# Kernel tuning notes

Hardware: AMD Instinct MI355X
Metric: run time of the kernel (lower is better)

The kernel has to match this reference:

```python
import jax, jax.numpy as jnp
import numpy as np

B, L, H = 32, 2048, 1024  # batch, seq (atoms), hid_dim; trg last dim = 3*H


def setup_inputs() -> dict:
    key = jax.random.key(0)
    k1, k2, k3, k4 = jax.random.split(key, 4)
    trg = jax.random.normal(k1, (B, L, 3 * H), dtype=jnp.float32)
    src = jax.random.normal(k2, (B, 512, H), dtype=jnp.float32)  # unused (n_layers=0)
    fc_w = jax.random.normal(k3, (H, 3 * H), dtype=jnp.float32) * (1.0 / np.sqrt(3 * H))
    fc_b = jax.random.normal(k4, (H,), dtype=jnp.float32) * 0.01
    return {"trg": trg, "src": src, "fc_w": fc_w, "fc_b": fc_b}


def reference(trg, src, fc_w, fc_b):
    # decoder layers: n_layers == 0 -> identity
    t = jnp.einsum('blk,hk->blh', trg, fc_w) + fc_b          # fc: [B, L, H]
    norm1 = jnp.linalg.norm(t, axis=2)                        # [B, L]
    w = jax.nn.softmax(norm1, axis=1)                         # [B, L]
    # vectorized form of the nested python-loop weighted-sum pooling
    summ = jnp.einsum('blh,bl->bh', t, w)                     # [B, H]
    return (summ, norm1)
```

## Files before the change

kernel.cpp:

```cpp
#include <hip/hip_runtime.h>
#include <hip/hip_bf16.h>


#define B_ 32
#define L_ 2048
#define H_ 1024
#define K_ 3072
#define M_ 65536

typedef __attribute__((ext_vector_type(8))) short short8;
typedef __attribute__((ext_vector_type(4))) float floatx4;

__device__ __forceinline__ unsigned int pack_bf16x2(float a, float b) {
    __hip_bfloat162 h = __float22bfloat162_rn(make_float2(a, b));
    return *reinterpret_cast<unsigned int*>(&h);
}

__device__ __forceinline__ float bf2f(unsigned short u) {
    return __uint_as_float(((unsigned int)u) << 16);
}

__device__ __forceinline__ void gl_lds16(const unsigned short* g, unsigned short* l) {
    __builtin_amdgcn_global_load_lds(
        (const __attribute__((address_space(1))) unsigned int*)g,
        (__attribute__((address_space(3))) unsigned int*)l, 16, 0, 0);
}

__global__ void __launch_bounds__(256) convert_bf16_kernel(const float* __restrict__ in,
                                                           unsigned short* __restrict__ out,
                                                           int n8) {
    int i = blockIdx.x * blockDim.x + threadIdx.x;
    const int stride = gridDim.x * blockDim.x;
    for (; i < n8; i += stride) {
        const float4* pp = (const float4*)in + (size_t)i * 2;
        float4 a = pp[0], b = pp[1];
        uint4 r;
        r.x = pack_bf16x2(a.x, a.y);
        r.y = pack_bf16x2(a.z, a.w);
        r.z = pack_bf16x2(b.x, b.y);
        r.w = pack_bf16x2(b.z, b.w);
        ((uint4*)out)[i] = r;
    }
}

__global__ void __launch_bounds__(256, 4) gemm_norm_bf_kernel(
        const unsigned short* __restrict__ A,
        const unsigned short* __restrict__ Bw,
        const float* __restrict__ fcb,
        float* __restrict__ normsq) {
    __shared__ unsigned short As[128 * 32];
    __shared__ unsigned short Bs[128 * 32];

    const int tid = threadIdx.x;
    const int bid = blockIdx.x;
    const int group  = bid >> 6;
    const int lane64 = bid & 63;
    const int xcd    = lane64 & 7;
    const int nblk   = lane64 >> 3;
    const int mblk   = group * 8 + xcd;
    const int R0 = mblk * 128;
    const int N0 = nblk * 128;

    const int wv = tid >> 6, lane = tid & 63;
    const int wr = wv >> 1, wc = wv & 1;
    const int q = lane >> 4, ln = lane & 15;

    const int r0    = wv * 32;
    const int lrow  = lane >> 2;
    const int lchnk = lane & 3;
    const unsigned short* agp = A  + (size_t)(R0 + r0 + lrow) * K_ + lchnk * 8;
    const unsigned short* bgp = Bw + (size_t)(N0 + r0 + lrow) * K_ + lchnk * 8;
    unsigned short* alds0 = &As[r0 * 32];
    unsigned short* alds1 = &As[(r0 + 16) * 32];
    unsigned short* blds0 = &Bs[r0 * 32];
    unsigned short* blds1 = &Bs[(r0 + 16) * 32];
    const size_t roff = (size_t)16 * K_;

    gl_lds16(agp, alds0);
    gl_lds16(agp + roff, alds1);
    gl_lds16(bgp, blds0);
    gl_lds16(bgp + roff, blds1);

    floatx4 acc[4][4] = {};
    const unsigned short* Af = &As[(wr * 64 + ln) * 32 + q * 8];
    const unsigned short* Bf = &Bs[(wc * 64 + ln) * 32 + q * 8];

    for (int step = 0; step < 96; ++step) {
        __syncthreads();

        short8 af[4], bf[4];
#pragma unroll
        for (int i = 0; i < 4; ++i) {
            af[i] = *(const short8*)(Af + i * 16 * 32);
            bf[i] = *(const short8*)(Bf + i * 16 * 32);
        }

        __syncthreads();

        if (step < 95) {
            const int kk = (step + 1) * 32;
            gl_lds16(agp + kk, alds0);
            gl_lds16(agp + roff + kk, alds1);
            gl_lds16(bgp + kk, blds0);
            gl_lds16(bgp + roff + kk, blds1);
        }

#pragma unroll
        for (int mi = 0; mi < 4; ++mi)
#pragma unroll
            for (int ni = 0; ni < 4; ++ni)
                acc[mi][ni] = __builtin_amdgcn_mfma_f32_16x16x32_bf16(af[mi], bf[ni],
                                                                      acc[mi][ni], 0, 0, 0);
    }

    float bz[4];
#pragma unroll
    for (int ni = 0; ni < 4; ++ni) bz[ni] = fcb[N0 + wc * 64 + ni * 16 + ln];

    float* nsq = normsq + R0 + wr * 64;
#pragma unroll
    for (int mi = 0; mi < 4; ++mi) {
#pragma unroll
        for (int r = 0; r < 4; ++r) {
            float s = 0.0f;
#pragma unroll
            for (int ni = 0; ni < 4; ++ni) {
                float v = acc[mi][ni][r] + bz[ni];
                s += v * v;
            }
            s += __shfl_xor(s, 1);
            s += __shfl_xor(s, 2);
            s += __shfl_xor(s, 4);
            s += __shfl_xor(s, 8);
            if (ln == 0) atomicAdd(&nsq[mi * 16 + q * 4 + r], s);
        }
    }
}

#define LDST 40
__global__ void __launch_bounds__(256) gemm_norm_f32_kernel(const float* __restrict__ trg,
                                                            const float* __restrict__ fcw,
                                                            const float* __restrict__ fcb,
                                                            float* __restrict__ normsq) {
    __shared__ unsigned short As[128 * LDST];
    __shared__ unsigned short Bs[128 * LDST];

    const int tid  = threadIdx.x;
    const int bid  = blockIdx.x;
    const int group  = bid >> 6;
    const int lane64 = bid & 63;
    const int nblk   = lane64 >> 3;
    const int mblk   = group * 8 + (lane64 & 7);
    const int R0   = mblk * 128;
    const int N0   = nblk * 128;
    const int wv   = tid >> 6;
    const int lane = tid & 63;
    const int wr   = wv >> 1;
    const int wc   = wv & 1;
    const int q    = lane >> 4;
    const int ln   = lane & 15;

    floatx4 acc[4][4] = {};

    const int srow = tid >> 3;
    const int skc  = tid & 7;
    const float* ap = trg + (size_t)(R0 + srow) * K_ + skc * 4;
    const float* bp = fcw + (size_t)(N0 + srow) * K_ + skc * 4;
    unsigned short* AsW = &As[srow * LDST + skc * 4];
    unsigned short* BsW = &Bs[srow * LDST + skc * 4];

    const unsigned short* Af = &As[(wr * 64 + ln) * LDST + q * 8];
    const unsigned short* Bf = &Bs[(wc * 64 + ln) * LDST + q * 8];

    float4 ra[4], rb[4];
#pragma unroll
    for (int s = 0; s < 4; ++s) {
        ra[s] = *(const float4*)(ap + (size_t)(s * 32) * K_);
        rb[s] = *(const float4*)(bp + (size_t)(s * 32) * K_);
    }

    for (int step = 0; step < 96; ++step) {
        __syncthreads();
#pragma unroll
        for (int s = 0; s < 4; ++s) {
            uint2 ua, ub;
            ua.x = pack_bf16x2(ra[s].x, ra[s].y);
            ua.y = pack_bf16x2(ra[s].z, ra[s].w);
            ub.x = pack_bf16x2(rb[s].x, rb[s].y);
            ub.y = pack_bf16x2(rb[s].z, rb[s].w);
            *(uint2*)(AsW + s * 32 * LDST) = ua;
            *(uint2*)(BsW + s * 32 * LDST) = ub;
        }
        if (step < 95) {
            const int kk = (step + 1) * 32;
#pragma unroll
            for (int s = 0; s < 4; ++s) {
                ra[s] = *(const float4*)(ap + (size_t)(s * 32) * K_ + kk);
                rb[s] = *(const float4*)(bp + (size_t)(s * 32) * K_ + kk);
            }
        }
        __syncthreads();

        short8 af[4], bf[4];
#pragma unroll
        for (int i = 0; i < 4; ++i) {
            af[i] = *(const short8*)(Af + i * 16 * LDST);
            bf[i] = *(const short8*)(Bf + i * 16 * LDST);
        }
#pragma unroll
        for (int mi = 0; mi < 4; ++mi)
#pragma unroll
            for (int ni = 0; ni < 4; ++ni)
                acc[mi][ni] = __builtin_amdgcn_mfma_f32_16x16x32_bf16(af[mi], bf[ni],
                                                                      acc[mi][ni], 0, 0, 0);
    }

    float bz[4];
#pragma unroll
    for (int ni = 0; ni < 4; ++ni) bz[ni] = fcb[N0 + wc * 64 + ni * 16 + ln];

    float* nsq = normsq + R0;
#pragma unroll
    for (int mi = 0; mi < 4; ++mi) {
#pragma unroll
        for (int r = 0; r < 4; ++r) {
            float s = 0.0f;
#pragma unroll
            for (int ni = 0; ni < 4; ++ni) {
                float v = acc[mi][ni][r] + bz[ni];
                s += v * v;
            }
            s += __shfl_xor(s, 1);
            s += __shfl_xor(s, 2);
            s += __shfl_xor(s, 4);
            s += __shfl_xor(s, 8);
            if (ln == 0) atomicAdd(&nsq[wr * 64 + mi * 16 + q * 4 + r], s);
        }
    }
}

__global__ void __launch_bounds__(256) softmax_stats_kernel(const float* __restrict__ normsq,
                                                            float* __restrict__ norm1,
                                                            float* __restrict__ bstats) {
    const int b = blockIdx.x;
    const int t = threadIdx.x;
    __shared__ float red[256];

    float vals[8];
    float mx = -1e30f;
#pragma unroll
    for (int i = 0; i < 8; ++i) {
        float v = sqrtf(normsq[b * L_ + i * 256 + t]);
        vals[i] = v;
        norm1[b * L_ + i * 256 + t] = v;
        mx = fmaxf(mx, v);
    }
    red[t] = mx;
    __syncthreads();
    for (int s = 128; s > 0; s >>= 1) {
        if (t < s) red[t] = fmaxf(red[t], red[t + s]);
        __syncthreads();
    }
    mx = red[0];
    __syncthreads();

    float sm = 0.0f;
#pragma unroll
    for (int i = 0; i < 8; ++i) sm += expf(vals[i] - mx);
    red[t] = sm;
    __syncthreads();
    for (int s = 128; s > 0; s >>= 1) {
        if (t < s) red[t] += red[t + s];
        __syncthreads();
    }
    if (t == 0) {
        bstats[b * 2 + 0] = mx;
        bstats[b * 2 + 1] = 1.0f / red[0];
    }
}

__global__ void __launch_bounds__(256) pool_bf_kernel(const unsigned short* __restrict__ trgbf,
                                                      const float* __restrict__ norm1,
                                                      const float* __restrict__ bstats,
                                                      float* __restrict__ p) {
    const int t  = threadIdx.x;
    const int b  = blockIdx.x / 48;
    const int r  = blockIdx.x % 48;
    const int lc = r / 3;
    const int kc = r % 3;
    const int l0 = lc * 128;

    __shared__ float wl[128];
    if (t < 128) {
        const float mx   = bstats[b * 2 + 0];
        const float sinv = bstats[b * 2 + 1];
        wl[t] = expf(norm1[b * L_ + l0 + t] - mx) * sinv;
    }
    __syncthreads();

    const int k = kc * 1024 + t * 4;
    const unsigned short* tp = trgbf + (size_t)(b * L_ + l0) * K_ + k;
    float4 acc = {0.0f, 0.0f, 0.0f, 0.0f};
    for (int i = 0; i < 128; ++i) {
        ushort4 v = *(const ushort4*)(tp + (size_t)i * K_);
        float w = wl[i];
        acc.x += w * bf2f(v.x);
        acc.y += w * bf2f(v.y);
        acc.z += w * bf2f(v.z);
        acc.w += w * bf2f(v.w);
    }
    float* pp = p + b * K_ + k;
    atomicAdd(&pp[0], acc.x);
    atomicAdd(&pp[1], acc.y);
    atomicAdd(&pp[2], acc.z);
    atomicAdd(&pp[3], acc.w);
}

__global__ void __launch_bounds__(256) pool_f32_kernel(const float* __restrict__ trg,
                                                       const float* __restrict__ norm1,
                                                       const float* __restrict__ bstats,
                                                       float* __restrict__ p) {
    const int t  = threadIdx.x;
    const int b  = blockIdx.x / 24;
    const int r  = blockIdx.x % 24;
    const int lc = r / 3;
    const int kc = r % 3;
    const int l0 = lc * 256;

    __shared__ float wl[256];
    const float mx   = bstats[b * 2 + 0];
    const float sinv = bstats[b * 2 + 1];
    wl[t] = expf(norm1[b * L_ + l0 + t] - mx) * sinv;
    __syncthreads();

    const int k = kc * 1024 + t * 4;
    const float* tp = trg + (size_t)b * L_ * K_ + (size_t)l0 * K_ + k;
    float4 acc = {0.0f, 0.0f, 0.0f, 0.0f};
    for (int i = 0; i < 256; ++i) {
        float4 v = *(const float4*)(tp + (size_t)i * K_);
        float w = wl[i];
        acc.x += w * v.x;
        acc.y += w * v.y;
        acc.z += w * v.z;
        acc.w += w * v.w;
    }
    float* pp = p + b * K_ + k;
    atomicAdd(&pp[0], acc.x);
    atomicAdd(&pp[1], acc.y);
    atomicAdd(&pp[2], acc.z);
    atomicAdd(&pp[3], acc.w);
}

__global__ void __launch_bounds__(256) summ_kernel(const float* __restrict__ fcw,
                                                   const float* __restrict__ fcb,
                                                   const float* __restrict__ p,
                                                   float* __restrict__ summ) {
    __shared__ float ps[K_];
    const int b  = blockIdx.x >> 2;
    const int hc = blockIdx.x & 3;
    const int t  = threadIdx.x;

    for (int i = t; i < K_ / 4; i += 256)
        ((float4*)ps)[i] = ((const float4*)(p + (size_t)b * K_))[i];
    __syncthreads();

    const int h = hc * 256 + t;
    const float4* wrow = (const float4*)(fcw + (size_t)h * K_);
    float acc = fcb[h];
    for (int i = 0; i < K_ / 4; ++i) {
        float4 wv = wrow[i];
        float4 pv = ((const float4*)ps)[i];
        acc += wv.x * pv.x + wv.y * pv.y + wv.z * pv.z + wv.w * pv.w;
    }
    summ[b * H_ + h] = acc;
}

extern "C" void kernel_launch(void* const* d_in, const int* in_sizes, int n_in,
                              void* d_out, int out_size, void* d_ws, size_t ws_size,
                              hipStream_t stream) {
    (void)in_sizes; (void)n_in; (void)out_size;
    const float* trg = (const float*)d_in[0];
    const float* fcw = (const float*)d_in[2];
    const float* fcb = (const float*)d_in[3];

    float* out   = (float*)d_out;
    float* summ  = out;
    float* norm1 = out + B_ * H_;

    const size_t trgbf_elems = (size_t)M_ * K_;
    const size_t fcwbf_elems = (size_t)H_ * K_;
    const size_t acc_bytes   = (size_t)(M_ + B_ * K_ + 64) * sizeof(float);
    const size_t need = (trgbf_elems + fcwbf_elems) * sizeof(unsigned short) + acc_bytes;

    if (ws_size >= need) {
        unsigned short* trgbf = (unsigned short*)d_ws;
        unsigned short* fcwbf = trgbf + trgbf_elems;
        float* normsq = (float*)(fcwbf + fcwbf_elems);
        float* p      = normsq + M_;
        float* bstats = p + B_ * K_;

        hipMemsetAsync(normsq, 0, acc_bytes, stream);
        hipLaunchKernelGGL(convert_bf16_kernel, dim3(16384), dim3(256), 0, stream,
                           trg, trgbf, (int)(trgbf_elems / 8));
        hipLaunchKernelGGL(convert_bf16_kernel, dim3(1536), dim3(256), 0, stream,
                           fcw, fcwbf, (int)(fcwbf_elems / 8));
        hipLaunchKernelGGL(gemm_norm_bf_kernel, dim3(4096), dim3(256), 0, stream,
                           trgbf, fcwbf, fcb, normsq);
        hipLaunchKernelGGL(softmax_stats_kernel, dim3(B_), dim3(256), 0, stream,
                           normsq, norm1, bstats);
        hipLaunchKernelGGL(pool_bf_kernel, dim3(B_ * 48), dim3(256), 0, stream,
                           trgbf, norm1, bstats, p);
        hipLaunchKernelGGL(summ_kernel, dim3(B_ * 4), dim3(256), 0, stream,
                           fcw, fcb, p, summ);
    } else {
        float* normsq = (float*)d_ws;
        float* p      = normsq + M_;
        float* bstats = p + B_ * K_;

        hipMemsetAsync(d_ws, 0, acc_bytes, stream);
        hipLaunchKernelGGL(gemm_norm_f32_kernel, dim3(4096), dim3(256), 0, stream,
                           trg, fcw, fcb, normsq);
        hipLaunchKernelGGL(softmax_stats_kernel, dim3(B_), dim3(256), 0, stream,
                           normsq, norm1, bstats);
        hipLaunchKernelGGL(pool_f32_kernel, dim3(B_ * 24), dim3(256), 0, stream,
                           trg, norm1, bstats, p);
        hipLaunchKernelGGL(summ_kernel, dim3(B_ * 4), dim3(256), 0, stream,
                           fcw, fcb, p, summ);
    }
}
```

Measured before the change: 1.762 ms.

## Restructure bf16 GEMM into 128x256 tiles with triple-buffered LDS pipeline

The main GEMM now uses 512-thread blocks computing 128x256 output tiles with a K-step of 64. The A tile is triple-buffered in LDS through async global-to-LDS loads with an XOR swizzle, and B fragments are loaded straight from global into double-buffered registers. A single barrier per step, explicit vmcnt waits and raised MFMA priority replace the previous two-barrier single-buffer loop, and the block-to-XCD mapping is changed. The aim is to overlap memory latency with MFMA work and cut synchronization per step, at the cost of higher register pressure and tricky wait-count correctness.

```diff
diff --git a/kernel.cpp b/kernel.cpp
--- a/kernel.cpp
+++ b/kernel.cpp
@@ -43,75 +43,122 @@
     }
 }
 
-__global__ void __launch_bounds__(256, 4) gemm_norm_bf_kernel(
+#define NT_ 48
+
+__global__ void __launch_bounds__(512, 2) gemm_norm_bf_kernel(
         const unsigned short* __restrict__ A,
         const unsigned short* __restrict__ Bw,
         const float* __restrict__ fcb,
         float* __restrict__ normsq) {
-    __shared__ unsigned short As[128 * 32];
-    __shared__ unsigned short Bs[128 * 32];
+    __shared__ unsigned short As[3 * 128 * 64];
 
     const int tid = threadIdx.x;
     const int bid = blockIdx.x;
-    const int group  = bid >> 6;
-    const int lane64 = bid & 63;
-    const int xcd    = lane64 & 7;
-    const int nblk   = lane64 >> 3;
-    const int mblk   = group * 8 + xcd;
+    const int xcd  = bid & 7;
+    const int seq  = bid >> 3;
+    const int mblk = xcd * 64 + (seq >> 2);
+    const int nblk = seq & 3;
     const int R0 = mblk * 128;
-    const int N0 = nblk * 128;
+    const int N0 = nblk * 256;
 
     const int wv = tid >> 6, lane = tid & 63;
-    const int wr = wv >> 1, wc = wv & 1;
+    const int wr = wv >> 2, wc = wv & 3;
     const int q = lane >> 4, ln = lane & 15;
 
-    const int r0    = wv * 32;
-    const int lrow  = lane >> 2;
-    const int lchnk = lane & 3;
-    const unsigned short* agp = A  + (size_t)(R0 + r0 + lrow) * K_ + lchnk * 8;
-    const unsigned short* bgp = Bw + (size_t)(N0 + r0 + lrow) * K_ + lchnk * 8;
-    unsigned short* alds0 = &As[r0 * 32];
-    unsigned short* alds1 = &As[(r0 + 16) * 32];
-    unsigned short* blds0 = &Bs[r0 * 32];
-    unsigned short* blds1 = &Bs[(r0 + 16) * 32];
-    const size_t roff = (size_t)16 * K_;
-
-    gl_lds16(agp, alds0);
-    gl_lds16(agp + roff, alds1);
-    gl_lds16(bgp, blds0);
-    gl_lds16(bgp + roff, blds1);
+    const int rin = lane >> 3;
+    const int slg = (lane & 7) ^ rin;
+    const unsigned short* ag0 = A + (size_t)(R0 + wv * 16 + rin) * K_ + slg * 8;
+    const unsigned short* ag1 = ag0 + (size_t)8 * K_;
+    unsigned short* al = As + wv * 1024;
+
+    const unsigned short* bg0 = Bw + (size_t)(N0 + wc * 64 + ln) * K_ + q * 8;
+    const unsigned short* bg1 = bg0 + (size_t)16 * K_;
+    const unsigned short* bg2 = bg0 + (size_t)32 * K_;
+    const unsigned short* bg3 = bg0 + (size_t)48 * K_;
+
+    const int arow = wr * 64 + ln;
+    const unsigned short* Af0 = As + arow * 64 + ((q ^ (ln & 7)) * 8);
+    const unsigned short* Af1 = As + arow * 64 + (((4 + q) ^ (ln & 7)) * 8);
 
     floatx4 acc[4][4] = {};
-    const unsigned short* Af = &As[(wr * 64 + ln) * 32 + q * 8];
-    const unsigned short* Bf = &Bs[(wc * 64 + ln) * 32 + q * 8];
-
-    for (int step = 0; step < 96; ++step) {
-        __syncthreads();
-
-        short8 af[4], bf[4];
-#pragma unroll
-        for (int i = 0; i < 4; ++i) {
-            af[i] = *(const short8*)(Af + i * 16 * 32);
-            bf[i] = *(const short8*)(Bf + i * 16 * 32);
-        }
-
-        __syncthreads();
-
-        if (step < 95) {
-            const int kk = (step + 1) * 32;
-            gl_lds16(agp + kk, alds0);
-            gl_lds16(agp + roff + kk, alds1);
-            gl_lds16(bgp + kk, blds0);
-            gl_lds16(bgp + roff + kk, blds1);
-        }
-
-#pragma unroll
-        for (int mi = 0; mi < 4; ++mi)
-#pragma unroll
-            for (int ni = 0; ni < 4; ++ni)
-                acc[mi][ni] = __builtin_amdgcn_mfma_f32_16x16x32_bf16(af[mi], bf[ni],
-                                                                      acc[mi][ni], 0, 0, 0);
-    }
+    short8 bf[2][4][2];
+
+    bf[0][0][0] = *(const short8*)(bg0);
+    bf[0][0][1] = *(const short8*)(bg0 + 32);
+    bf[0][1][0] = *(const short8*)(bg1);
+    bf[0][1][1] = *(const short8*)(bg1 + 32);
+    bf[0][2][0] = *(const short8*)(bg2);
+    bf[0][2][1] = *(const short8*)(bg2 + 32);
+    bf[0][3][0] = *(const short8*)(bg3);
+    bf[0][3][1] = *(const short8*)(bg3 + 32);
+    __builtin_amdgcn_sched_barrier(0);
+    gl_lds16(ag0, al);
+    gl_lds16(ag1, al + 512);
+    gl_lds16(ag0 + 64, al + 8192);
+    gl_lds16(ag1 + 64, al + 8192 + 512);
+    __builtin_amdgcn_sched_barrier(0);
+
+#define MFMA4(MI, AV, KKI)                                                              \
+    acc[MI][0] = __builtin_amdgcn_mfma_f32_16x16x32_bf16(AV, bf[cur][0][KKI], acc[MI][0], 0, 0, 0); \
+    acc[MI][1] = __builtin_amdgcn_mfma_f32_16x16x32_bf16(AV, bf[cur][1][KKI], acc[MI][1], 0, 0, 0); \
+    acc[MI][2] = __builtin_amdgcn_mfma_f32_16x16x32_bf16(AV, bf[cur][2][KKI], acc[MI][2], 0, 0, 0); \
+    acc[MI][3] = __builtin_amdgcn_mfma_f32_16x16x32_bf16(AV, bf[cur][3][KKI], acc[MI][3], 0, 0, 0);
+
+    for (int it = 0; it < 8; ++it) {
+#pragma unroll
+        for (int u = 0; u < 6; ++u) {
+            const int t   = it * 6 + u;
+            const int buf = u % 3;
+            const int cur = u & 1;
+            const int nxt = cur ^ 1;
+
+            asm volatile("s_waitcnt vmcnt(2)" ::: "memory");
+            __builtin_amdgcn_s_barrier();
+
+            if (t < 47) {
+                const int ko = (t + 1) * 64;
+                bf[nxt][0][0] = *(const short8*)(bg0 + ko);
+                bf[nxt][0][1] = *(const short8*)(bg0 + ko + 32);
+                bf[nxt][1][0] = *(const short8*)(bg1 + ko);
+                bf[nxt][1][1] = *(const short8*)(bg1 + ko + 32);
+                bf[nxt][2][0] = *(const short8*)(bg2 + ko);
+                bf[nxt][2][1] = *(const short8*)(bg2 + ko + 32);
+                bf[nxt][3][0] = *(const short8*)(bg3 + ko);
+                bf[nxt][3][1] = *(const short8*)(bg3 + ko + 32);
+            }
+            __builtin_amdgcn_sched_barrier(0);
+
+            if (t < 46) gl_lds16(ag0 + (t + 2) * 64, al + ((u + 2) % 3) * 8192);
+            {
+                const unsigned short* af = Af0 + buf * 8192;
+                short8 a0 = *(const short8*)(af);
+                short8 a1 = *(const short8*)(af + 1024);
+                short8 a2 = *(const short8*)(af + 2048);
+                short8 a3 = *(const short8*)(af + 3072);
+                __builtin_amdgcn_s_setprio(1);
+                MFMA4(0, a0, 0)
+                MFMA4(1, a1, 0)
+                MFMA4(2, a2, 0)
+                MFMA4(3, a3, 0)
+                __builtin_amdgcn_s_setprio(0);
+            }
+            if (t < 46) gl_lds16(ag1 + (t + 2) * 64, al + ((u + 2) % 3) * 8192 + 512);
+            {
+                const unsigned short* af = Af1 + buf * 8192;
+                short8 a0 = *(const short8*)(af);
+                short8 a1 = *(const short8*)(af + 1024);
+                short8 a2 = *(const short8*)(af + 2048);
+                short8 a3 = *(const short8*)(af + 3072);
+                __builtin_amdgcn_s_setprio(1);
+                MFMA4(0, a0, 1)
+                MFMA4(1, a1, 1)
+                MFMA4(2, a2, 1)
+                MFMA4(3, a3, 1)
+                __builtin_amdgcn_s_setprio(0);
+            }
+        }
+    }
+#undef MFMA4
 
     float bz[4];
 #pragma unroll
@@ -201,17 +248,17 @@
         }
         __syncthreads();
 
-        short8 af[4], bf[4];
+        short8 af[4], bfr[4];
 #pragma unroll
         for (int i = 0; i < 4; ++i) {
-            af[i] = *(const short8*)(Af + i * 16 * LDST);
-            bf[i] = *(const short8*)(Bf + i * 16 * LDST);
+            af[i]  = *(const short8*)(Af + i * 16 * LDST);
+            bfr[i] = *(const short8*)(Bf + i * 16 * LDST);
         }
 #pragma unroll
         for (int mi = 0; mi < 4; ++mi)
 #pragma unroll
             for (int ni = 0; ni < 4; ++ni)
-                acc[mi][ni] = __builtin_amdgcn_mfma_f32_16x16x32_bf16(af[mi], bf[ni],
+                acc[mi][ni] = __builtin_amdgcn_mfma_f32_16x16x32_bf16(af[mi], bfr[ni],
                                                                       acc[mi][ni], 0, 0, 0);
     }
 
@@ -404,7 +451,7 @@
                            trg, trgbf, (int)(trgbf_elems / 8));
         hipLaunchKernelGGL(convert_bf16_kernel, dim3(1536), dim3(256), 0, stream,
                            fcw, fcwbf, (int)(fcwbf_elems / 8));
-        hipLaunchKernelGGL(gemm_norm_bf_kernel, dim3(4096), dim3(256), 0, stream,
+        hipLaunchKernelGGL(gemm_norm_bf_kernel, dim3(2048), dim3(512), 0, stream,
                            trgbf, fcwbf, fcb, normsq);
         hipLaunchKernelGGL(softmax_stats_kernel, dim3(B_), dim3(256), 0, stream,
                            normsq, norm1, bstats);
```

New measurement: 2.195 ms. 24.6% more time.

## Double the GEMM K-tile to 64 with XOR-swizzled LDS layout

Applied to the files above, without the earlier changes.

Widens the bf16 GEMM K tile from 32 to 64, which halves the number of main-loop iterations and barriers. The LDS layout gets an XOR swizzle on the 16-byte chunk index, applied both when loading from global and when reading MFMA fragments, to avoid bank conflicts on the wider rows. The two halves of the K slice are computed in sequence, and the next tile's loads are issued after the second fragment read so they overlap the second MFMA batch. LDS use per block doubles, which may reduce occupancy. A variable rename in the second kernel is cosmetic.

```diff
diff --git a/kernel.cpp b/kernel.cpp
--- a/kernel.cpp
+++ b/kernel.cpp
@@ -48,8 +48,8 @@
         const unsigned short* __restrict__ Bw,
         const float* __restrict__ fcb,
         float* __restrict__ normsq) {
-    __shared__ unsigned short As[128 * 32];
-    __shared__ unsigned short Bs[128 * 32];
+    __shared__ unsigned short As[128 * 64];
+    __shared__ unsigned short Bs[128 * 64];
 
     const int tid = threadIdx.x;
     const int bid = blockIdx.x;
@@ -65,51 +65,65 @@
     const int wr = wv >> 1, wc = wv & 1;
     const int q = lane >> 4, ln = lane & 15;
 
-    const int r0    = wv * 32;
-    const int lrow  = lane >> 2;
-    const int lchnk = lane & 3;
-    const unsigned short* agp = A  + (size_t)(R0 + r0 + lrow) * K_ + lchnk * 8;
-    const unsigned short* bgp = Bw + (size_t)(N0 + r0 + lrow) * K_ + lchnk * 8;
-    unsigned short* alds0 = &As[r0 * 32];
-    unsigned short* alds1 = &As[(r0 + 16) * 32];
-    unsigned short* blds0 = &Bs[r0 * 32];
-    unsigned short* blds1 = &Bs[(r0 + 16) * 32];
-    const size_t roff = (size_t)16 * K_;
-
-    gl_lds16(agp, alds0);
-    gl_lds16(agp + roff, alds1);
-    gl_lds16(bgp, blds0);
-    gl_lds16(bgp + roff, blds1);
+    const int rin = lane >> 3;
+    const int slg = (lane & 7) ^ rin;
+    const unsigned short* agp = A  + (size_t)(R0 + wv * 32 + rin) * K_ + slg * 8;
+    const unsigned short* bgp = Bw + (size_t)(N0 + wv * 32 + rin) * K_ + slg * 8;
+    unsigned short* alds = &As[wv * 32 * 64];
+    unsigned short* blds = &Bs[wv * 32 * 64];
+
+    const int sw = ln & 7;
+    const unsigned short* Af0 = &As[(wr * 64 + ln) * 64 + ((q ^ sw) * 8)];
+    const unsigned short* Af1 = &As[(wr * 64 + ln) * 64 + (((4 + q) ^ sw) * 8)];
+    const unsigned short* Bf0 = &Bs[(wc * 64 + ln) * 64 + ((q ^ sw) * 8)];
+    const unsigned short* Bf1 = &Bs[(wc * 64 + ln) * 64 + (((4 + q) ^ sw) * 8)];
 
     floatx4 acc[4][4] = {};
-    const unsigned short* Af = &As[(wr * 64 + ln) * 32 + q * 8];
-    const unsigned short* Bf = &Bs[(wc * 64 + ln) * 32 + q * 8];
-
-    for (int step = 0; step < 96; ++step) {
-        __syncthreads();
-
-        short8 af[4], bf[4];
+
+#pragma unroll
+    for (int j = 0; j < 4; ++j) {
+        gl_lds16(agp + (size_t)(j * 8) * K_, alds + j * 512);
+        gl_lds16(bgp + (size_t)(j * 8) * K_, blds + j * 512);
+    }
+
+    for (int step = 0; step < 48; ++step) {
+        __syncthreads();
+
+        short8 a0[4], b0[4];
 #pragma unroll
         for (int i = 0; i < 4; ++i) {
-            af[i] = *(const short8*)(Af + i * 16 * 32);
-            bf[i] = *(const short8*)(Bf + i * 16 * 32);
-        }
-
-        __syncthreads();
-
-        if (step < 95) {
-            const int kk = (step + 1) * 32;
-            gl_lds16(agp + kk, alds0);
-            gl_lds16(agp + roff + kk, alds1);
-            gl_lds16(bgp + kk, blds0);
-            gl_lds16(bgp + roff + kk, blds1);
-        }
-
+            a0[i] = *(const short8*)(Af0 + i * 1024);
+            b0[i] = *(const short8*)(Bf0 + i * 1024);
+        }
 #pragma unroll
         for (int mi = 0; mi < 4; ++mi)
 #pragma unroll
             for (int ni = 0; ni < 4; ++ni)
-                acc[mi][ni] = __builtin_amdgcn_mfma_f32_16x16x32_bf16(af[mi], bf[ni],
+                acc[mi][ni] = __builtin_amdgcn_mfma_f32_16x16x32_bf16(a0[mi], b0[ni],
+                                                                      acc[mi][ni], 0, 0, 0);
+
+        short8 a1[4], b1[4];
+#pragma unroll
+        for (int i = 0; i < 4; ++i) {
+            a1[i] = *(const short8*)(Af1 + i * 1024);
+            b1[i] = *(const short8*)(Bf1 + i * 1024);
+        }
+        __syncthreads();
+
+        if (step < 47) {
+            const int kb = (step + 1) * 64;
+#pragma unroll
+            for (int j = 0; j < 4; ++j) {
+                gl_lds16(agp + (size_t)(j * 8) * K_ + kb, alds + j * 512);
+                gl_lds16(bgp + (size_t)(j * 8) * K_ + kb, blds + j * 512);
+            }
+        }
+
+#pragma unroll
+        for (int mi = 0; mi < 4; ++mi)
+#pragma unroll
+            for (int ni = 0; ni < 4; ++ni)
+                acc[mi][ni] = __builtin_amdgcn_mfma_f32_16x16x32_bf16(a1[mi], b1[ni],
                                                                       acc[mi][ni], 0, 0, 0);
     }
 
@@ -201,17 +215,17 @@
         }
         __syncthreads();
 
-        short8 af[4], bf[4];
+        short8 af[4], bfr[4];
 #pragma unroll
         for (int i = 0; i < 4; ++i) {
-            af[i] = *(const short8*)(Af + i * 16 * LDST);
-            bf[i] = *(const short8*)(Bf + i * 16 * LDST);
+            af[i]  = *(const short8*)(Af + i * 16 * LDST);
+            bfr[i] = *(const short8*)(Bf + i * 16 * LDST);
         }
 #pragma unroll
         for (int mi = 0; mi < 4; ++mi)
 #pragma unroll
             for (int ni = 0; ni < 4; ++ni)
-                acc[mi][ni] = __builtin_amdgcn_mfma_f32_16x16x32_bf16(af[mi], bf[ni],
+                acc[mi][ni] = __builtin_amdgcn_mfma_f32_16x16x32_bf16(af[mi], bfr[ni],
                                                                       acc[mi][ni], 0, 0, 0);
     }
 
```

After: 1.664 ms. 1.06x faster.
